# Optimization experiments

Measured on AMD Instinct MI355X. Metric: run time of the kernel, lower is better.

The kernel has to match this reference:

```python
import jax, jax.numpy as jnp
import numpy as np

HIDDEN = 3072
HEADS = 24
HEAD_DIM = HIDDEN // HEADS  # 128
MLP_HIDDEN = 4 * HIDDEN     # 12288
EPS = 1e-6


def rotate_half(x):
    # interleaved pairs: (x1, x2) -> (-x2, x1)
    xr = x.reshape(*x.shape[:-1], -1, 2)
    x1, x2 = xr[..., 0], xr[..., 1]
    return jnp.stack((-x2, x1), axis=-1).reshape(x.shape)


def rms_norm(x, gamma):
    var = jnp.mean(x * x, axis=-1, keepdims=True)
    return x * jax.lax.rsqrt(var + EPS) * gamma


def layer_norm(x):
    mu = jnp.mean(x, axis=-1, keepdims=True)
    var = jnp.mean(jnp.square(x - mu), axis=-1, keepdims=True)
    return (x - mu) * jax.lax.rsqrt(var + EPS)


def setup_inputs() -> dict:
    key = jax.random.key(0)
    ks = jax.random.split(key, 8)
    B, L_IMG, TXT = 2, 1024, 256
    L = L_IMG + TXT
    s = 0.02
    x = jax.random.normal(ks[0], (B, L, HIDDEN), jnp.float32)
    vec = jax.random.normal(ks[1], (B, HIDDEN), jnp.float32)
    w1 = jax.random.normal(ks[2], (HIDDEN, 3 * HIDDEN + MLP_HIDDEN), jnp.float32) * s
    b1 = jnp.zeros((3 * HIDDEN + MLP_HIDDEN,), jnp.float32)
    w2 = jax.random.normal(ks[3], (HIDDEN + MLP_HIDDEN, HIDDEN), jnp.float32) * s
    b2 = jnp.zeros((HIDDEN,), jnp.float32)
    wmod = jax.random.normal(ks[4], (HIDDEN, 3 * HIDDEN), jnp.float32) * s
    bmod = jnp.zeros((3 * HIDDEN,), jnp.float32)
    q_gamma = jnp.ones((HEAD_DIM,), jnp.float32)
    k_gamma = jnp.ones((HEAD_DIM,), jnp.float32)
    # real RoPE tables for the image tokens
    inv_freq = 1.0 / (10000.0 ** (np.arange(0, HEAD_DIM, 2, dtype=np.float32) / HEAD_DIM))
    angles = np.arange(L_IMG, dtype=np.float32)[:, None] * inv_freq[None, :]  # [L_img, D/2]
    freqs_cos = jnp.asarray(np.repeat(np.cos(angles), 2, axis=-1))  # [L_img, D]
    freqs_sin = jnp.asarray(np.repeat(np.sin(angles), 2, axis=-1))
    cu_seqlens_q = jnp.asarray([0, L, L, 2 * L, 2 * L], jnp.int32)  # no padding
    return {"x": x, "vec": vec, "w1": w1, "b1": b1, "w2": w2, "b2": b2,
            "wmod": wmod, "bmod": bmod, "q_gamma": q_gamma, "k_gamma": k_gamma,
            "freqs_cos": freqs_cos, "freqs_sin": freqs_sin,
            "txt_len": TXT, "cu_seqlens_q": cu_seqlens_q}


def reference(x, vec, w1, b1, w2, b2, wmod, bmod, q_gamma, k_gamma,
              freqs_cos, freqs_sin, txt_len, cu_seqlens_q):
    B, L, _ = x.shape
    # modulation: SiLU(vec) @ Wmod -> shift/scale/gate
    mod = jax.nn.silu(vec) @ wmod + bmod              # [B, 3H]
    mod_shift, mod_scale, mod_gate = jnp.split(mod, 3, axis=-1)
    x_mod = layer_norm(x) * (1.0 + mod_scale[:, None, :]) + mod_shift[:, None, :]
    h = x_mod @ w1 + b1                               # [B, L, 3H + mlp]
    qkv, mlp = h[..., :3 * HIDDEN], h[..., 3 * HIDDEN:]
    qkv = qkv.reshape(B, L, 3, HEADS, HEAD_DIM)
    q, k, v = qkv[:, :, 0], qkv[:, :, 1], qkv[:, :, 2]  # [B, L, H, D]
    q = rms_norm(q, q_gamma)
    k = rms_norm(k, k_gamma)
    # RoPE on image tokens (first L - txt_len)
    cos = freqs_cos[None, :, None, :]
    sin = freqs_sin[None, :, None, :]
    img_q, txt_q = q[:, :-txt_len], q[:, -txt_len:]
    img_k, txt_k = k[:, :-txt_len], k[:, -txt_len:]
    img_q = img_q * cos + rotate_half(img_q) * sin
    img_k = img_k * cos + rotate_half(img_k) * sin
    q = jnp.concatenate((img_q, txt_q), axis=1)
    k = jnp.concatenate((img_k, txt_k), axis=1)
    # full attention (no padding => each batch is one varlen segment)
    scale = HEAD_DIM ** -0.5
    scores = jnp.einsum("bqhd,bkhd->bhqk", q, k) * scale
    probs = jax.nn.softmax(scores, axis=-1)
    attn = jnp.einsum("bhqk,bkhd->bqhd", probs, v).reshape(B, L, HIDDEN)
    out = jnp.concatenate((attn, jax.nn.gelu(mlp, approximate=True)), axis=-1) @ w2 + b2
    return x + out * mod_gate[:, None, :]
```

## Files before the change

kernel.cpp:

```cpp
#include <hip/hip_runtime.h>

typedef unsigned short u16;
typedef unsigned int   u32;
typedef __attribute__((ext_vector_type(2))) u16 u16x2;
typedef __attribute__((ext_vector_type(4))) u16 u16x4;
typedef __attribute__((ext_vector_type(8))) u16 u16x8;
typedef __attribute__((ext_vector_type(8))) __bf16 bf16x8;
typedef __attribute__((ext_vector_type(4))) float f32x4;

#define HIDDEN 3072
#define LTOT 1280
#define BATCH 2
#define NROWS (BATCH*LTOT)
#define HEADS 24
#define HD 128
#define N1 21504
#define QKVW 9216
#define MLPW 12288
#define A2W 15360
#define EPSF 1e-6f

__device__ __forceinline__ float b2f(u16 u) {
  union { u32 i; float f; } v; v.i = ((u32)u) << 16; return v.f;
}
__device__ __forceinline__ u16 f2b(float f) {
  union { float f; u32 i; } v; v.f = f;
  u32 r = (v.i + 0x7FFFu + ((v.i >> 16) & 1u)) >> 16;
  return (u16)r;
}
__device__ __forceinline__ float lde(const void* p, size_t i, int f) {
  return f ? b2f(((const u16*)p)[i]) : ((const float*)p)[i];
}
__device__ __forceinline__ void gload16(const void* g, void* l) {
  __builtin_amdgcn_global_load_lds((const __attribute__((address_space(1))) void*)g,
                                   (__attribute__((address_space(3))) void*)l, 16, 0, 0);
}
__device__ __forceinline__ bf16x8 ldf(const u16* p) {
  return __builtin_bit_cast(bf16x8, *(const u16x8*)p);
}
__device__ __forceinline__ float gelu_tanh(float x) {
  float u = 0.7978845608028654f * (x + 0.044715f * x * x * x);
  float e = __expf(2.0f * u);
  float th = 1.0f - 2.0f / (e + 1.0f);
  return 0.5f * x * (1.0f + th);
}

__global__ void detect_kernel(const u16* __restrict__ fcos, int* __restrict__ dflag) {
  if (threadIdx.x == 0 && blockIdx.x == 0) *dflag = (fcos[0] == 0x3F80) ? 1 : 0;
}

__global__ void silu_kernel(const void* __restrict__ vec, float* __restrict__ sv,
                            const int* __restrict__ dflag) {
  int flag = *dflag;
  int i = blockIdx.x * 256 + threadIdx.x;
  if (i < BATCH * HIDDEN) { float x = lde(vec, i, flag); sv[i] = x / (1.0f + __expf(-x)); }
}

__global__ void modmul(const void* __restrict__ wmod, const float* __restrict__ sv,
                       float* __restrict__ modp, const int* __restrict__ dflag) {
  int flag = *dflag;
  int j = blockIdx.x * 256 + threadIdx.x;
  int kc = blockIdx.y;
  float a = 0.f, c = 0.f;
  int k0 = kc * 384;
  for (int k = k0; k < k0 + 384; ++k) {
    float w = lde(wmod, (size_t)k * QKVW + j, flag);
    a += sv[k] * w; c += sv[HIDDEN + k] * w;
  }
  modp[(size_t)kc * 2 * QKVW + j] = a;
  modp[(size_t)kc * 2 * QKVW + QKVW + j] = c;
}

__global__ void modred(const float* __restrict__ modp, const void* __restrict__ bmod,
                       float* __restrict__ mod, const int* __restrict__ dflag) {
  int flag = *dflag;
  int j = blockIdx.x * 256 + threadIdx.x;
  float bv = lde(bmod, j, flag);
  float a = bv, c = bv;
#pragma unroll
  for (int kc = 0; kc < 8; ++kc) {
    a += modp[(size_t)kc * 2 * QKVW + j];
    c += modp[(size_t)kc * 2 * QKVW + QKVW + j];
  }
  mod[j] = a; mod[QKVW + j] = c;
}

__global__ __launch_bounds__(256) void ln_mod_kernel(const void* __restrict__ x,
                                                     const float* __restrict__ mod,
                                                     u16* __restrict__ xmod,
                                                     const int* __restrict__ dflag) {
  int flag = *dflag;
  int row = blockIdx.x;
  int b = row / LTOT;
  int t = threadIdx.x, w = t >> 6, l = t & 63;
  float v[12], sum = 0.0f, sq = 0.0f;
  if (flag) {
    const u16* xr = (const u16*)x + (size_t)row * HIDDEN;
#pragma unroll
    for (int p = 0; p < 3; ++p) {
      u16x4 u = *(const u16x4*)&xr[p * 1024 + t * 4];
#pragma unroll
      for (int i = 0; i < 4; ++i) { float f = b2f(u[i]); v[p * 4 + i] = f; sum += f; sq += f * f; }
    }
  } else {
    const float* xr = (const float*)x + (size_t)row * HIDDEN;
#pragma unroll
    for (int p = 0; p < 3; ++p) {
      f32x4 u = *(const f32x4*)&xr[p * 1024 + t * 4];
#pragma unroll
      for (int i = 0; i < 4; ++i) { float f = u[i]; v[p * 4 + i] = f; sum += f; sq += f * f; }
    }
  }
#pragma unroll
  for (int off = 1; off < 64; off <<= 1) { sum += __shfl_xor(sum, off, 64); sq += __shfl_xor(sq, off, 64); }
  __shared__ float red[2][4];
  if (l == 0) { red[0][w] = sum; red[1][w] = sq; }
  __syncthreads();
  sum = red[0][0] + red[0][1] + red[0][2] + red[0][3];
  sq  = red[1][0] + red[1][1] + red[1][2] + red[1][3];
  float mu = sum / (float)HIDDEN;
  float var = sq / (float)HIDDEN - mu * mu;
  float rs = rsqrtf(var + EPSF);
  const float* mb = mod + (size_t)b * QKVW;
#pragma unroll
  for (int p = 0; p < 3; ++p) {
    u16x4 o;
#pragma unroll
    for (int i = 0; i < 4; ++i) {
      int col = p * 1024 + t * 4 + i;
      float y = (v[p * 4 + i] - mu) * rs;
      o[i] = f2b(y * (1.0f + mb[HIDDEN + col]) + mb[col]);
    }
    *(u16x4*)&xmod[(size_t)row * HIDDEN + p * 1024 + t * 4] = o;
  }
}

__global__ void transpose_cvt(const void* __restrict__ in, u16* __restrict__ out,
                              int R, int C, const int* __restrict__ dflag) {
  int flag = *dflag;
  __shared__ u16 tile[32][33];
  int bx = blockIdx.x * 32, by = blockIdx.y * 32;
  int tx = threadIdx.x & 31, ty = threadIdx.x >> 5;
#pragma unroll
  for (int i = 0; i < 32; i += 8)
    tile[ty + i][tx] = f2b(lde(in, (size_t)(by + ty + i) * C + bx + tx, flag));
  __syncthreads();
#pragma unroll
  for (int i = 0; i < 32; i += 8) out[(size_t)(bx + ty + i) * R + by + tx] = tile[tx][ty + i];
}

__global__ void transpose_bf16(const u16* __restrict__ in, u16* __restrict__ out,
                               int R, int C, size_t ibs, size_t obs) {
  in  += (size_t)blockIdx.z * ibs;
  out += (size_t)blockIdx.z * obs;
  __shared__ u16 tile[32][33];
  int bx = blockIdx.x * 32, by = blockIdx.y * 32;
  int tx = threadIdx.x & 31, ty = threadIdx.x >> 5;
#pragma unroll
  for (int i = 0; i < 32; i += 8) tile[ty + i][tx] = in[(size_t)(by + ty + i) * C + bx + tx];
  __syncthreads();
#pragma unroll
  for (int i = 0; i < 32; i += 8) out[(size_t)(bx + ty + i) * R + by + tx] = tile[tx][ty + i];
}

__global__ __launch_bounds__(512, 2) void gemm1_p3(
    const u16* __restrict__ A, const u16* __restrict__ Bt,
    const void* __restrict__ bias,
    u16* __restrict__ Qb, u16* __restrict__ Kb, u16* __restrict__ Vb,
    u16* __restrict__ A2, const int* __restrict__ dflag) {
  __shared__ u16 As[3][256][32];
  __shared__ u16 Bs[3][256][32];
  constexpr int K = HIDDEN;
  constexpr int NT = K / 32;
  const int tid = threadIdx.x;
  const int l = tid & 63, w = tid >> 6;
  const int wr = w >> 2, wc = w & 3;
  const int lr = l & 15, g = l >> 4;
  const int lk_sw = (g ^ ((lr >> 1) & 3)) * 8;

  const int orig = blockIdx.x;
  const int wgid = (orig & 7) * 105 + (orig >> 3);
  const int my = wgid / 84, nx = wgid - my * 84;
  const int bm = my * 256, bn = nx * 256;

  const int row_s = tid >> 2, chunk = tid & 3;
  const int c_log = chunk ^ ((row_s >> 1) & 3);
  const u16* pa = A  + (size_t)(bm + row_s) * K + c_log * 8;
  const u16* pb = Bt + (size_t)(bn + row_s) * K + c_log * 8;

  auto stage_a = [&](int buf, int t) {
    const u16* sa = pa + t * 32;
    u16* la = &As[buf][row_s][chunk * 8];
    gload16(sa,                   la);
    gload16(sa + (size_t)128 * K, la + 128 * 32);
  };
  auto stage_b = [&](int buf, int t) {
    const u16* sb = pb + t * 32;
    u16* lb = &Bs[buf][row_s][chunk * 8];
    gload16(sb,                   lb);
    gload16(sb + (size_t)128 * K, lb + 128 * 32);
  };

  f32x4 acc[8][4] = {};

  stage_a(0, 0); stage_b(0, 0);
  stage_a(1, 1); stage_b(1, 1);
  stage_a(2, 2); stage_b(2, 2);
  asm volatile("s_waitcnt vmcnt(8)" ::: "memory");
  __builtin_amdgcn_s_barrier();

  bf16x8 af[4], bfr[4];
  for (int t = 0; t < NT; ++t) {
    const int buf = t % 3;
    const int buf2 = (t + 2) % 3;
    const bool pre = (t + 2 < NT);

#pragma unroll
    for (int fc = 0; fc < 4; ++fc) bfr[fc] = ldf(&Bs[buf][wc * 64 + fc * 16 + lr][lk_sw]);
#pragma unroll
    for (int j = 0; j < 4; ++j) af[j] = ldf(&As[buf][wr * 128 + j * 16 + lr][lk_sw]);
    if (pre) stage_a(buf2, t + 2);
    __builtin_amdgcn_s_barrier();
    asm volatile("s_waitcnt lgkmcnt(0)" ::: "memory");
    __builtin_amdgcn_sched_barrier(0);
    __builtin_amdgcn_s_setprio(1);
#pragma unroll
    for (int j = 0; j < 4; ++j)
#pragma unroll
      for (int fc = 0; fc < 4; ++fc)
        acc[j][fc] = __builtin_amdgcn_mfma_f32_16x16x32_bf16(af[j], bfr[fc], acc[j][fc], 0, 0, 0);
    __builtin_amdgcn_s_setprio(0);
    __builtin_amdgcn_s_barrier();

#pragma unroll
    for (int j = 0; j < 4; ++j) af[j] = ldf(&As[buf][wr * 128 + (4 + j) * 16 + lr][lk_sw]);
    if (pre) {
      stage_b(buf2, t + 2);
      asm volatile("s_waitcnt vmcnt(4)" ::: "memory");
    } else if (t + 1 < NT) {
      asm volatile("s_waitcnt vmcnt(0)" ::: "memory");
    }
    __builtin_amdgcn_s_barrier();
    asm volatile("s_waitcnt lgkmcnt(0)" ::: "memory");
    __builtin_amdgcn_sched_barrier(0);
    __builtin_amdgcn_s_setprio(1);
#pragma unroll
    for (int j = 0; j < 4; ++j)
#pragma unroll
      for (int fc = 0; fc < 4; ++fc)
        acc[4 + j][fc] = __builtin_amdgcn_mfma_f32_16x16x32_bf16(af[j], bfr[fc], acc[4 + j][fc], 0, 0, 0);
    __builtin_amdgcn_s_setprio(0);
    __builtin_amdgcn_s_barrier();
  }

  const int flag = *dflag;
#pragma unroll
  for (int fr = 0; fr < 8; ++fr) {
#pragma unroll
    for (int fc = 0; fc < 4; ++fc) {
      int colg = bn + wc * 64 + fc * 16 + lr;
      float bv = lde(bias, colg, flag);
#pragma unroll
      for (int r = 0; r < 4; ++r) {
        int rowg = bm + wr * 128 + fr * 16 + g * 4 + r;
        float v = acc[fr][fc][r] + bv;
        if (colg < QKVW) {
          int which = colg / HIDDEN;
          int hd = colg - which * HIDDEN;
          int h = hd >> 7, d = hd & 127;
          int b2 = rowg / LTOT, pos = rowg - b2 * LTOT;
          u16* dst = (which == 0) ? Qb : ((which == 1) ? Kb : Vb);
          dst[(((size_t)(b2 * HEADS + h)) * LTOT + pos) * HD + d] = f2b(v);
        } else {
          A2[(size_t)rowg * A2W + HIDDEN + (colg - QKVW)] = f2b(gelu_tanh(v));
        }
      }
    }
  }
}

template <int MODE>
__global__ __launch_bounds__(256) void gemm_bt(
    const u16* __restrict__ A, const u16* __restrict__ Bt, int K,
    const void* __restrict__ bias,
    u16* __restrict__ out0, u16* __restrict__ out1, u16* __restrict__ out2,
    u16* __restrict__ out3, float* __restrict__ outf,
    const void* __restrict__ xin, const float* __restrict__ mod,
    const int* __restrict__ dflag) {
  __shared__ u16 As[128 * 32];
  __shared__ u16 Bs[128 * 32];
  const int flag = *dflag;
  const int t = threadIdx.x;
  const int bn = blockIdx.x * 128;
  const int bm = blockIdx.y * 128;
  const int w = t >> 6, l = t & 63;
  const int wr = (w >> 1) * 64, wc = (w & 1) * 64;
  const int lr = l & 15, lk = (l >> 4) * 8;
  f32x4 acc[4][4] = {};
  const size_t a_base = (size_t)bm * K;
  const size_t b_base = (size_t)bn * K;
  const int e0 = t * 8, e1 = e0 + 2048;
  const int r0 = e0 >> 5, c0 = e0 & 31;
  const int r1 = e1 >> 5, c1 = e1 & 31;
  const int nk = K / 32;
  for (int kt = 0; kt < nk; ++kt) {
    const int k0 = kt * 32;
    __syncthreads();
    gload16(A + a_base + (size_t)r0 * K + k0 + c0, (u16*)As + e0);
    gload16(A + a_base + (size_t)r1 * K + k0 + c1, (u16*)As + e1);
    gload16(Bt + b_base + (size_t)r0 * K + k0 + c0, (u16*)Bs + e0);
    gload16(Bt + b_base + (size_t)r1 * K + k0 + c1, (u16*)Bs + e1);
    __syncthreads();
    bf16x8 af[4], bfr[4];
#pragma unroll
    for (int i = 0; i < 4; ++i) {
      af[i]  = __builtin_bit_cast(bf16x8, *(const u16x8*)&As[(wr + i * 16 + lr) * 32 + lk]);
      bfr[i] = __builtin_bit_cast(bf16x8, *(const u16x8*)&Bs[(wc + i * 16 + lr) * 32 + lk]);
    }
#pragma unroll
    for (int i = 0; i < 4; ++i)
#pragma unroll
      for (int j = 0; j < 4; ++j)
        acc[i][j] = __builtin_amdgcn_mfma_f32_16x16x32_bf16(af[i], bfr[j], acc[i][j], 0, 0, 0);
  }
#pragma unroll
  for (int i = 0; i < 4; ++i) {
#pragma unroll
    for (int j = 0; j < 4; ++j) {
      int colg = bn + wc + j * 16 + lr;
      float bv = lde(bias, colg, flag);
#pragma unroll
      for (int r = 0; r < 4; ++r) {
        int rowg = bm + wr + i * 16 + (l >> 4) * 4 + r;
        float v = acc[i][j][r] + bv;
        if (MODE == 1) {
        } else {
          int b = rowg / LTOT;
          float gg = mod[(size_t)b * QKVW + 2 * HIDDEN + colg];
          float xv = lde(xin, (size_t)rowg * HIDDEN + colg, flag);
          outf[(size_t)rowg * HIDDEN + colg] = xv + v * gg;
        }
      }
    }
  }
}

__global__ __launch_bounds__(256) void rms_rope(
    u16* __restrict__ Qb, u16* __restrict__ Kb,
    const void* __restrict__ qg, const void* __restrict__ kg,
    const void* __restrict__ fcos, const void* __restrict__ fsin,
    const int* __restrict__ dflag) {
  int flag = *dflag;
  int w = threadIdx.x >> 6, l = threadIdx.x & 63;
  int rid = blockIdx.x * 4 + w;
  int pos = rid % LTOT;
  int d0 = 2 * l;
  size_t off = (size_t)rid * HD + d0;
  u16x2 qu = *(const u16x2*)&Qb[off];
  u16x2 ku = *(const u16x2*)&Kb[off];
  float q0 = b2f(qu[0]), q1 = b2f(qu[1]);
  float k0 = b2f(ku[0]), k1 = b2f(ku[1]);
  float sq = q0 * q0 + q1 * q1, sk = k0 * k0 + k1 * k1;
#pragma unroll
  for (int o = 1; o < 64; o <<= 1) { sq += __shfl_xor(sq, o, 64); sk += __shfl_xor(sk, o, 64); }
  float rq = rsqrtf(sq / 128.0f + EPSF), rk = rsqrtf(sk / 128.0f + EPSF);
  q0 *= rq * lde(qg, d0, flag); q1 *= rq * lde(qg, d0 + 1, flag);
  k0 *= rk * lde(kg, d0, flag); k1 *= rk * lde(kg, d0 + 1, flag);
  if (pos < 1024) {
    float cc = lde(fcos, (size_t)pos * HD + d0, flag);
    float ss = lde(fsin, (size_t)pos * HD + d0, flag);
    float nq0 = q0 * cc - q1 * ss, nq1 = q1 * cc + q0 * ss;
    float nk0 = k0 * cc - k1 * ss, nk1 = k1 * cc + k0 * ss;
    q0 = nq0; q1 = nq1; k0 = nk0; k1 = nk1;
  }
  u16x2 qo; qo[0] = f2b(q0); qo[1] = f2b(q1);
  u16x2 ko; ko[0] = f2b(k0); ko[1] = f2b(k1);
  *(u16x2*)&Qb[off] = qo;
  *(u16x2*)&Kb[off] = ko;
}

__global__ __launch_bounds__(256) void attn_kernel(
    const u16* __restrict__ Qb, const u16* __restrict__ Kb, const u16* __restrict__ Vt,
    u16* __restrict__ A2) {
  __shared__ u16 Ks[32 * 128];
  __shared__ u16 Vs[128 * 32];
  __shared__ u16 Ps[4][512];
  int t = threadIdx.x, w = t >> 6, l = t & 63;
  int bh = blockIdx.y;
  int q0 = blockIdx.x * 64 + w * 16;
  size_t base = (size_t)bh * LTOT * HD;
  int lr = l & 15, lk = (l >> 4) * 8;
  const float scale = 0.08838834764831845f;

  bf16x8 qf[4];
#pragma unroll
  for (int c = 0; c < 4; ++c)
    qf[c] = __builtin_bit_cast(bf16x8, *(const u16x8*)&Qb[base + (size_t)(q0 + lr) * HD + c * 32 + lk]);

  f32x4 o[8] = {};
  float mrun[4] = {-1e30f, -1e30f, -1e30f, -1e30f};
  float lrun[4] = {0.f, 0.f, 0.f, 0.f};

  const int e0 = t * 8, e1 = e0 + 2048;
  const int vd0 = e0 >> 5, vc0 = e0 & 31;
  const int vd1 = e1 >> 5, vc1 = e1 & 31;

  for (int kt = 0; kt < LTOT / 32; ++kt) {
    __syncthreads();
    gload16(Kb + base + (size_t)kt * 32 * HD + e0, (u16*)Ks + e0);
    gload16(Kb + base + (size_t)kt * 32 * HD + e1, (u16*)Ks + e1);
    gload16(Vt + base + (size_t)vd0 * LTOT + kt * 32 + vc0, (u16*)Vs + e0);
    gload16(Vt + base + (size_t)vd1 * LTOT + kt * 32 + vc1, (u16*)Vs + e1);
    __syncthreads();

    f32x4 s[2] = {};
#pragma unroll
    for (int sb = 0; sb < 2; ++sb)
#pragma unroll
      for (int c = 0; c < 4; ++c) {
        bf16x8 kf = __builtin_bit_cast(bf16x8, *(const u16x8*)&Ks[(sb * 16 + lr) * 128 + c * 32 + lk]);
        s[sb] = __builtin_amdgcn_mfma_f32_16x16x32_bf16(qf[c], kf, s[sb], 0, 0, 0);
      }
#pragma unroll
    for (int sb = 0; sb < 2; ++sb)
#pragma unroll
      for (int j = 0; j < 4; ++j) s[sb][j] *= scale;

#pragma unroll
    for (int j = 0; j < 4; ++j) {
      float mt = fmaxf(s[0][j], s[1][j]);
#pragma unroll
      for (int off = 1; off < 16; off <<= 1) mt = fmaxf(mt, __shfl_xor(mt, off, 64));
      float mnew = fmaxf(mrun[j], mt);
      float f = __expf(mrun[j] - mnew);
      float p0 = __expf(s[0][j] - mnew), p1 = __expf(s[1][j] - mnew);
      float ps = p0 + p1;
#pragma unroll
      for (int off = 1; off < 16; off <<= 1) ps += __shfl_xor(ps, off, 64);
      lrun[j] = lrun[j] * f + ps;
      mrun[j] = mnew;
#pragma unroll
      for (int nb = 0; nb < 8; ++nb) o[nb][j] *= f;
      int prow = (l >> 4) * 4 + j;
      Ps[w][prow * 32 + lr] = f2b(p0);
      Ps[w][prow * 32 + 16 + lr] = f2b(p1);
    }
    __syncthreads();
    bf16x8 pa = __builtin_bit_cast(bf16x8, *(const u16x8*)&Ps[w][lr * 32 + lk]);
#pragma unroll
    for (int nb = 0; nb < 8; ++nb) {
      bf16x8 vf = __builtin_bit_cast(bf16x8, *(const u16x8*)&Vs[(nb * 16 + lr) * 32 + lk]);
      o[nb] = __builtin_amdgcn_mfma_f32_16x16x32_bf16(pa, vf, o[nb], 0, 0, 0);
    }
  }

  int b = bh / HEADS, h = bh % HEADS;
#pragma unroll
  for (int j = 0; j < 4; ++j) {
    float inv = 1.0f / lrun[j];
    size_t row = (size_t)b * LTOT + q0 + (l >> 4) * 4 + j;
#pragma unroll
    for (int nb = 0; nb < 8; ++nb) {
      int col = h * HD + nb * 16 + lr;
      A2[row * A2W + col] = f2b(o[nb][j] * inv);
    }
  }
}

extern "C" void kernel_launch(void* const* d_in, const int* in_sizes, int n_in,
                              void* d_out, int out_size, void* d_ws, size_t ws_size,
                              hipStream_t stream) {
  const void* x    = d_in[0];
  const void* vec  = d_in[1];
  const void* w1   = d_in[2];
  const void* b1   = d_in[3];
  const void* w2   = d_in[4];
  const void* b2   = d_in[5];
  const void* wmod = d_in[6];
  const void* bmod = d_in[7];
  const void* qg   = d_in[8];
  const void* kg   = d_in[9];
  const void* fcos = d_in[10];
  const void* fsin = d_in[11];

  char* p = (char*)d_ws;
  int* dflag  = (int*)p; p += 256;
  float* sv   = (float*)p; p += 32768;
  float* mod  = (float*)p; p += 131072;
  float* modp = (float*)p; p += 8 * 2 * QKVW * 4;
  u16* xmod = (u16*)p; p += (size_t)NROWS * HIDDEN * 2;
  u16* w1t  = (u16*)p; p += (size_t)N1 * HIDDEN * 2;
  u16* Qb   = (u16*)p; p += (size_t)48 * LTOT * HD * 2;
  u16* Kb   = (u16*)p; p += (size_t)48 * LTOT * HD * 2;
  u16* Vb   = (u16*)p; p += (size_t)48 * LTOT * HD * 2;
  u16* Vt   = (u16*)p; p += (size_t)48 * LTOT * HD * 2;
  u16* A2   = (u16*)p; p += (size_t)NROWS * A2W * 2;
  u16* w2t  = w1t;

  detect_kernel<<<1, 64, 0, stream>>>((const u16*)fcos, dflag);
  silu_kernel<<<24, 256, 0, stream>>>(vec, sv, dflag);
  modmul<<<dim3(36, 8), 256, 0, stream>>>(wmod, sv, modp, dflag);
  modred<<<36, 256, 0, stream>>>(modp, bmod, mod, dflag);
  ln_mod_kernel<<<NROWS, 256, 0, stream>>>(x, mod, xmod, dflag);
  transpose_cvt<<<dim3(N1 / 32, HIDDEN / 32), 256, 0, stream>>>(w1, w1t, HIDDEN, N1, dflag);
  gemm1_p3<<<(N1 / 256) * (NROWS / 256), 512, 0, stream>>>(xmod, w1t, b1,
                                                           Qb, Kb, Vb, A2, dflag);
  rms_rope<<<48 * LTOT / 4, 256, 0, stream>>>(Qb, Kb, qg, kg, fcos, fsin, dflag);
  transpose_bf16<<<dim3(HD / 32, LTOT / 32, 48), 256, 0, stream>>>(Vb, Vt, LTOT, HD,
                                                                   (size_t)LTOT * HD, (size_t)LTOT * HD);
  attn_kernel<<<dim3(LTOT / 64, 48), 256, 0, stream>>>(Qb, Kb, Vt, A2);
  transpose_cvt<<<dim3(HIDDEN / 32, A2W / 32), 256, 0, stream>>>(w2, w2t, A2W, HIDDEN, dflag);
  gemm_bt<2><<<dim3(HIDDEN / 128, NROWS / 128), 256, 0, stream>>>(A2, w2t, A2W, b2,
                                                                  nullptr, nullptr, nullptr, nullptr,
                                                                  (float*)d_out, x, mod, dflag);
}
```

Baseline: 1.477 ms.

## Replace second GEMM with pipelined 256x256 split-K kernel plus reduce epilogue

Swaps the simple 128x128 single-buffered output GEMM for a 256x256-tile, 3-stage LDS-pipelined kernel modeled on gemm1. It splits K in two across 240 blocks with grouped tile ordering, writes fp32 partial sums into the reused Q/K buffer, and adds a separate reduce kernel that applies bias, gate and residual. The first GEMM's prologue is also changed to prefetch only two stages. The cost is an extra fp32 partial-sum round trip through memory and one more launch.

Result: faster. 1.317 ms (-10.8%).

```diff
diff --git a/kernel.cpp b/kernel.cpp
--- a/kernel.cpp
+++ b/kernel.cpp
@@ -205,8 +205,7 @@
 
   stage_a(0, 0); stage_b(0, 0);
   stage_a(1, 1); stage_b(1, 1);
-  stage_a(2, 2); stage_b(2, 2);
-  asm volatile("s_waitcnt vmcnt(8)" ::: "memory");
+  asm volatile("s_waitcnt vmcnt(4)" ::: "memory");
   __builtin_amdgcn_s_barrier();
 
   bf16x8 af[4], bfr[4];
@@ -279,70 +278,129 @@
   }
 }
 
-template <int MODE>
-__global__ __launch_bounds__(256) void gemm_bt(
-    const u16* __restrict__ A, const u16* __restrict__ Bt, int K,
-    const void* __restrict__ bias,
-    u16* __restrict__ out0, u16* __restrict__ out1, u16* __restrict__ out2,
-    u16* __restrict__ out3, float* __restrict__ outf,
-    const void* __restrict__ xin, const float* __restrict__ mod,
-    const int* __restrict__ dflag) {
-  __shared__ u16 As[128 * 32];
-  __shared__ u16 Bs[128 * 32];
-  const int flag = *dflag;
-  const int t = threadIdx.x;
-  const int bn = blockIdx.x * 128;
-  const int bm = blockIdx.y * 128;
-  const int w = t >> 6, l = t & 63;
-  const int wr = (w >> 1) * 64, wc = (w & 1) * 64;
-  const int lr = l & 15, lk = (l >> 4) * 8;
-  f32x4 acc[4][4] = {};
-  const size_t a_base = (size_t)bm * K;
-  const size_t b_base = (size_t)bn * K;
-  const int e0 = t * 8, e1 = e0 + 2048;
-  const int r0 = e0 >> 5, c0 = e0 & 31;
-  const int r1 = e1 >> 5, c1 = e1 & 31;
-  const int nk = K / 32;
-  for (int kt = 0; kt < nk; ++kt) {
-    const int k0 = kt * 32;
-    __syncthreads();
-    gload16(A + a_base + (size_t)r0 * K + k0 + c0, (u16*)As + e0);
-    gload16(A + a_base + (size_t)r1 * K + k0 + c1, (u16*)As + e1);
-    gload16(Bt + b_base + (size_t)r0 * K + k0 + c0, (u16*)Bs + e0);
-    gload16(Bt + b_base + (size_t)r1 * K + k0 + c1, (u16*)Bs + e1);
-    __syncthreads();
-    bf16x8 af[4], bfr[4];
-#pragma unroll
-    for (int i = 0; i < 4; ++i) {
-      af[i]  = __builtin_bit_cast(bf16x8, *(const u16x8*)&As[(wr + i * 16 + lr) * 32 + lk]);
-      bfr[i] = __builtin_bit_cast(bf16x8, *(const u16x8*)&Bs[(wc + i * 16 + lr) * 32 + lk]);
-    }
-#pragma unroll
-    for (int i = 0; i < 4; ++i)
-#pragma unroll
-      for (int j = 0; j < 4; ++j)
-        acc[i][j] = __builtin_amdgcn_mfma_f32_16x16x32_bf16(af[i], bfr[j], acc[i][j], 0, 0, 0);
-  }
+__global__ __launch_bounds__(512, 2) void gemm2_p3(
+    const u16* __restrict__ A, const u16* __restrict__ Bt,
+    float* __restrict__ psum) {
+  __shared__ u16 As[3][256][32];
+  __shared__ u16 Bs[3][256][32];
+  constexpr int K = A2W;
+  constexpr int NT = 7680 / 32;
+  const int tid = threadIdx.x;
+  const int l = tid & 63, w = tid >> 6;
+  const int wr = w >> 2, wc = w & 3;
+  const int lr = l & 15, g = l >> 4;
+  const int lk_sw = (g ^ ((lr >> 1) & 3)) * 8;
+
+  const int s = blockIdx.y;
+  const int orig = blockIdx.x;
+  const int wgid = (orig & 7) * 15 + (orig >> 3);
+  const int my = wgid / 12, nx = wgid - my * 12;
+  const int bm = my * 256, bn = nx * 256;
+  const int kbase = s * 7680;
+
+  const int row_s = tid >> 2, chunk = tid & 3;
+  const int c_log = chunk ^ ((row_s >> 1) & 3);
+  const u16* pa = A  + (size_t)(bm + row_s) * K + kbase + c_log * 8;
+  const u16* pb = Bt + (size_t)(bn + row_s) * K + kbase + c_log * 8;
+
+  auto stage_a = [&](int buf, int t) {
+    const u16* sa = pa + t * 32;
+    u16* la = &As[buf][row_s][chunk * 8];
+    gload16(sa,                   la);
+    gload16(sa + (size_t)128 * K, la + 128 * 32);
+  };
+  auto stage_b = [&](int buf, int t) {
+    const u16* sb = pb + t * 32;
+    u16* lb = &Bs[buf][row_s][chunk * 8];
+    gload16(sb,                   lb);
+    gload16(sb + (size_t)128 * K, lb + 128 * 32);
+  };
+
+  f32x4 acc[8][4] = {};
+
+  stage_a(0, 0); stage_b(0, 0);
+  stage_a(1, 1); stage_b(1, 1);
+  asm volatile("s_waitcnt vmcnt(4)" ::: "memory");
+  __builtin_amdgcn_s_barrier();
+
+  bf16x8 af[4], bfr[4];
+  for (int t = 0; t < NT; ++t) {
+    const int buf = t % 3;
+    const int buf2 = (t + 2) % 3;
+    const bool pre = (t + 2 < NT);
+
+#pragma unroll
+    for (int fc = 0; fc < 4; ++fc) bfr[fc] = ldf(&Bs[buf][wc * 64 + fc * 16 + lr][lk_sw]);
+#pragma unroll
+    for (int j = 0; j < 4; ++j) af[j] = ldf(&As[buf][wr * 128 + j * 16 + lr][lk_sw]);
+    if (pre) stage_a(buf2, t + 2);
+    __builtin_amdgcn_s_barrier();
+    asm volatile("s_waitcnt lgkmcnt(0)" ::: "memory");
+    __builtin_amdgcn_sched_barrier(0);
+    __builtin_amdgcn_s_setprio(1);
+#pragma unroll
+    for (int j = 0; j < 4; ++j)
+#pragma unroll
+      for (int fc = 0; fc < 4; ++fc)
+        acc[j][fc] = __builtin_amdgcn_mfma_f32_16x16x32_bf16(af[j], bfr[fc], acc[j][fc], 0, 0, 0);
+    __builtin_amdgcn_s_setprio(0);
+    __builtin_amdgcn_s_barrier();
+
+#pragma unroll
+    for (int j = 0; j < 4; ++j) af[j] = ldf(&As[buf][wr * 128 + (4 + j) * 16 + lr][lk_sw]);
+    if (pre) {
+      stage_b(buf2, t + 2);
+      asm volatile("s_waitcnt vmcnt(4)" ::: "memory");
+    } else if (t + 1 < NT) {
+      asm volatile("s_waitcnt vmcnt(0)" ::: "memory");
+    }
+    __builtin_amdgcn_s_barrier();
+    asm volatile("s_waitcnt lgkmcnt(0)" ::: "memory");
+    __builtin_amdgcn_sched_barrier(0);
+    __builtin_amdgcn_s_setprio(1);
+#pragma unroll
+    for (int j = 0; j < 4; ++j)
+#pragma unroll
+      for (int fc = 0; fc < 4; ++fc)
+        acc[4 + j][fc] = __builtin_amdgcn_mfma_f32_16x16x32_bf16(af[j], bfr[fc], acc[4 + j][fc], 0, 0, 0);
+    __builtin_amdgcn_s_setprio(0);
+    __builtin_amdgcn_s_barrier();
+  }
+
+  float* pout = psum + (size_t)s * NROWS * HIDDEN;
+#pragma unroll
+  for (int fr = 0; fr < 8; ++fr) {
+#pragma unroll
+    for (int fc = 0; fc < 4; ++fc) {
+      int colg = bn + wc * 64 + fc * 16 + lr;
+#pragma unroll
+      for (int r = 0; r < 4; ++r) {
+        int rowg = bm + wr * 128 + fr * 16 + g * 4 + r;
+        pout[(size_t)rowg * HIDDEN + colg] = acc[fr][fc][r];
+      }
+    }
+  }
+}
+
+__global__ __launch_bounds__(256) void gemm2_reduce(
+    const float* __restrict__ psum, const void* __restrict__ bias,
+    const float* __restrict__ mod, const void* __restrict__ xin,
+    float* __restrict__ outf, const int* __restrict__ dflag) {
+  int flag = *dflag;
+  int col = blockIdx.x * 1024 + threadIdx.x * 4;
+  int row = blockIdx.y;
+  int b = row / LTOT;
+  f32x4 v0 = *(const f32x4*)&psum[(size_t)row * HIDDEN + col];
+  f32x4 v1 = *(const f32x4*)&psum[((size_t)NROWS + row) * HIDDEN + col];
+  f32x4 o;
 #pragma unroll
   for (int i = 0; i < 4; ++i) {
-#pragma unroll
-    for (int j = 0; j < 4; ++j) {
-      int colg = bn + wc + j * 16 + lr;
-      float bv = lde(bias, colg, flag);
-#pragma unroll
-      for (int r = 0; r < 4; ++r) {
-        int rowg = bm + wr + i * 16 + (l >> 4) * 4 + r;
-        float v = acc[i][j][r] + bv;
-        if (MODE == 1) {
-        } else {
-          int b = rowg / LTOT;
-          float gg = mod[(size_t)b * QKVW + 2 * HIDDEN + colg];
-          float xv = lde(xin, (size_t)rowg * HIDDEN + colg, flag);
-          outf[(size_t)rowg * HIDDEN + colg] = xv + v * gg;
-        }
-      }
-    }
-  }
+    float gg = mod[(size_t)b * QKVW + 2 * HIDDEN + col + i];
+    float bv = lde(bias, col + i, flag);
+    float xv = lde(xin, (size_t)row * HIDDEN + col + i, flag);
+    o[i] = xv + (v0[i] + v1[i] + bv) * gg;
+  }
+  *(f32x4*)&outf[(size_t)row * HIDDEN + col] = o;
 }
 
 __global__ __launch_bounds__(256) void rms_rope(
@@ -496,6 +554,7 @@
   u16* Vt   = (u16*)p; p += (size_t)48 * LTOT * HD * 2;
   u16* A2   = (u16*)p; p += (size_t)NROWS * A2W * 2;
   u16* w2t  = w1t;
+  float* psum = (float*)Qb;
 
   detect_kernel<<<1, 64, 0, stream>>>((const u16*)fcos, dflag);
   silu_kernel<<<24, 256, 0, stream>>>(vec, sv, dflag);
@@ -510,7 +569,6 @@
                                                                    (size_t)LTOT * HD, (size_t)LTOT * HD);
   attn_kernel<<<dim3(LTOT / 64, 48), 256, 0, stream>>>(Qb, Kb, Vt, A2);
   transpose_cvt<<<dim3(HIDDEN / 32, A2W / 32), 256, 0, stream>>>(w2, w2t, A2W, HIDDEN, dflag);
-  gemm_bt<2><<<dim3(HIDDEN / 128, NROWS / 128), 256, 0, stream>>>(A2, w2t, A2W, b2,
-                                                                  nullptr, nullptr, nullptr, nullptr,
-                                                                  (float*)d_out, x, mod, dflag);
-}
+  gemm2_p3<<<dim3(120, 2), 512, 0, stream>>>(A2, w2t, psum);
+  gemm2_reduce<<<dim3(3, NROWS), 256, 0, stream>>>(psum, b2, mod, x, (float*)d_out, dflag);
+}
```
